# Kernel tuning notes

Hardware: AMD Instinct MI355X
Metric: run time of the kernel (lower is better)

The kernel has to match this reference:

```python
import math
import jax, jax.numpy as jnp
import numpy as np

EMB = 1024
HEADS = 16
HD = EMB // HEADS  # 64
MAXPOS = 1024
BATCH = 4
SEQ = 1024


def get_rope_cache(dim, max_pos, theta=10000.0):
    # NOTE: faithfully reproduces the (i - 1) quirk of the source (not the standard i)
    i = jnp.arange(dim // 2, dtype=jnp.float32)
    theta_i = theta ** (-2.0 * (i - 1.0) / dim)
    pos = jnp.arange(max_pos, dtype=jnp.float32)[:, None]
    th = pos * theta_i  # [max_pos, dim//2]
    return jnp.stack([jnp.cos(th), jnp.sin(th)], axis=-1)  # [max_pos, dim//2, 2]


def apply_rope(x, rope_cache):
    # x: [B, H, S, hd]. Source casts pairs to float16 before the complex multiply,
    # then the complex32*complex64 product promotes back to float32 -> emulate via
    # an fp16 round-trip on x, with the rotation itself done in fp32.
    B, H, S, hd = x.shape
    rc = rope_cache[:S]  # [S, hd//2, 2]
    xp = x.reshape(B, H, S, hd // 2, 2).astype(jnp.float16).astype(jnp.float32)
    a, b = xp[..., 0], xp[..., 1]
    cos, sin = rc[..., 0], rc[..., 1]
    rot = jnp.stack([a * cos - b * sin, a * sin + b * cos], axis=-1)
    return rot.reshape(B, H, S, hd)


def setup_inputs() -> dict:
    key = jax.random.key(0)
    ks = jax.random.split(key, 5)
    std = math.sqrt(2.0 / (EMB + EMB))
    x = jax.random.normal(ks[0], (BATCH, SEQ, EMB), dtype=jnp.float32)
    padding_mask = jnp.ones((BATCH, SEQ), dtype=jnp.float32)
    Wq = jax.random.normal(ks[1], (EMB, EMB), dtype=jnp.float32) * std
    Wk = jax.random.normal(ks[2], (EMB, EMB), dtype=jnp.float32) * std
    Wv = jax.random.normal(ks[3], (EMB, EMB), dtype=jnp.float32) * std
    Wo = jax.random.normal(ks[4], (EMB, EMB), dtype=jnp.float32) * std
    rope_cache = get_rope_cache(HD, MAXPOS)
    return {"x": x, "padding_mask": padding_mask, "Wq": Wq, "Wk": Wk,
            "Wv": Wv, "Wo": Wo, "rope_cache": rope_cache}


def reference(x, padding_mask, Wq, Wk, Wv, Wo, rope_cache):
    B, S, E = x.shape

    def heads(t):  # [B,S,E] -> [B,H,S,hd]
        return t.reshape(B, S, HEADS, HD).transpose(0, 2, 1, 3)

    q = heads(x @ Wq.T)
    k = heads(x @ Wk.T)
    v = heads(x @ Wv.T)
    q = apply_rope(q, rope_cache)
    k = apply_rope(k, rope_cache)

    scores = jnp.einsum('bhqd,bhkd->bhqk', q, k)  # [B,H,S,S]
    causal = jnp.tril(jnp.ones((S, S), jnp.float32))
    mask = (causal[None, :, :] * padding_mask[:, None, :])[:, None]  # [B,1,S,S]
    scores = jnp.where(mask == 0, jnp.float32(-1e9), scores) / math.sqrt(HD)
    weights = jax.nn.softmax(scores, axis=-1)

    out = jnp.einsum('bhqk,bhkd->bhqd', weights, v)  # [B,H,S,hd]
    # Faithful to source: transpose(-2,-1) then .view(B,S,-1) scrambles head_dim/seq
    out = out.transpose(0, 1, 3, 2).reshape(B, S, E)
    return out @ Wo.T
```

## Files before the change

### kernel.cpp

```cpp
#include <hip/hip_runtime.h>

#define SEQ   1024
#define HEADS 16
#define HD    64
#define BATCH 4
#define EMB   1024

typedef __attribute__((ext_vector_type(8))) short  short8;
typedef __attribute__((ext_vector_type(4))) float  floatx4;

__device__ __forceinline__ unsigned short f2bf(float f) {
    unsigned u = __builtin_bit_cast(unsigned, f);
    u += 0x7FFF + ((u >> 16) & 1);
    return (unsigned short)(u >> 16);
}

__device__ __forceinline__ void g2l16(const void* g, void* l) {
    __builtin_amdgcn_global_load_lds((const __attribute__((address_space(1))) unsigned int*)g,
                                     (__attribute__((address_space(3))) unsigned int*)l,
                                     16, 0, 0);
}

__device__ __forceinline__ short8 ldsfrag(const unsigned short* base, int row, int cq) {
    int ch = cq ^ (row & 7);
    return *(const short8*)(base + row * 64 + ch * 8);
}

__global__ __launch_bounds__(256) void cvt_kernel(
    const float* __restrict__ x,  const float* __restrict__ wq,
    const float* __restrict__ wk, const float* __restrict__ wv,
    const float* __restrict__ wo,
    unsigned short* __restrict__ xb,  unsigned short* __restrict__ wqb,
    unsigned short* __restrict__ wkb, unsigned short* __restrict__ wvb,
    unsigned short* __restrict__ wob) {
    int blk = blockIdx.x;
    const float* src; unsigned short* dst; int rel;
    if      (blk < 4096) { src = x;  dst = xb;  rel = blk; }
    else if (blk < 5120) { src = wq; dst = wqb; rel = blk - 4096; }
    else if (blk < 6144) { src = wk; dst = wkb; rel = blk - 5120; }
    else if (blk < 7168) { src = wv; dst = wvb; rel = blk - 6144; }
    else                 { src = wo; dst = wob; rel = blk - 7168; }
    size_t i = (size_t)rel * 1024 + threadIdx.x * 4;
    float4 v = *(const float4*)(src + i);
    ushort4 o;
    o.x = f2bf(v.x); o.y = f2bf(v.y); o.z = f2bf(v.z); o.w = f2bf(v.w);
    *(ushort4*)(dst + i) = o;
}

template<int MODE>
__global__ __launch_bounds__(256) void gemm_m97(
    const unsigned short* __restrict__ A, const unsigned short* __restrict__ W,
    void* __restrict__ out0, void* __restrict__ out1, void* __restrict__ out2,
    const float* __restrict__ rc, int M, int N, int K) {
    __shared__ unsigned short As[2][128 * 64];
    __shared__ unsigned short Bs[2][128 * 64];
    const int tid  = threadIdx.x;
    const int lane = tid & 63;
    const int wid  = tid >> 6;
    const int l15  = lane & 15, quad = lane >> 4;
    const int wm   = (wid & 1) * 64, wn = (wid >> 1) * 64;
    const int m0   = blockIdx.y * 128, n0 = blockIdx.x * 128;
    const int boff = tid * 16;

    floatx4 acc[4][4] = {};
    const char* Ab = (const char*)A;
    const char* Wb = (const char*)W;
    const size_t rstride = (size_t)K * 2;

    auto stageStep = [&](int bufi, int k0) {
#pragma unroll
        for (int c = 0; c < 4; c++) {
            int o = c * 4096 + boff;
            int row = o >> 7;
            int sw  = ((o >> 4) & 7) ^ (row & 7);
            g2l16(Ab + (size_t)(m0 + row) * rstride + (size_t)k0 * 2 + sw * 16,
                  (char*)As[bufi] + o);
            g2l16(Wb + (size_t)(n0 + row) * rstride + (size_t)k0 * 2 + sw * 16,
                  (char*)Bs[bufi] + o);
        }
    };

    stageStep(0, 0);
    __syncthreads();

    int cur = 0;
    for (int k0 = 0; k0 < K; k0 += 64) {
        if (k0 + 64 < K) stageStep(cur ^ 1, k0 + 64);

        const unsigned short* Ac = As[cur];
        const unsigned short* Bc = Bs[cur];
#pragma unroll
        for (int ks = 0; ks < 2; ks++) {
            short8 a[4], b[4];
#pragma unroll
            for (int i = 0; i < 4; i++) a[i] = ldsfrag(Ac, wm + i * 16 + l15, ks * 4 + quad);
#pragma unroll
            for (int j = 0; j < 4; j++) b[j] = ldsfrag(Bc, wn + j * 16 + l15, ks * 4 + quad);
#pragma unroll
            for (int i = 0; i < 4; i++)
#pragma unroll
                for (int j = 0; j < 4; j++)
                    acc[i][j] = __builtin_amdgcn_mfma_f32_16x16x32_bf16(a[i], b[j], acc[i][j], 0, 0, 0);
        }

        asm volatile("s_waitcnt vmcnt(0)" ::: "memory");
        __syncthreads();
        cur ^= 1;
    }

    const int which = n0 >> 10;
#pragma unroll
    for (int i = 0; i < 4; i++) {
#pragma unroll
        for (int r = 0; r < 4; r++) {
            int m = m0 + wm + i * 16 + quad * 4 + r;
            int bb = m >> 10, s = m & 1023;
#pragma unroll
            for (int j = 0; j < 4; j++) {
                int n = n0 + wn + j * 16 + l15;
                float v = acc[i][j][r];
                if (MODE == 0) {
                    ((float*)out0)[(size_t)m * N + n] = v;
                } else {
                    int nr = n & 1023, h = nr >> 6, d = nr & 63;
                    if (which < 2) {
                        float vp = __shfl_xor(v, 1);
                        float2 cs = *(const float2*)&rc[(size_t)s * 64 + (d & ~1)];
                        v = (l15 & 1) ? (vp * cs.y + v * cs.x) : (v * cs.x - vp * cs.y);
                        unsigned short* dst = (which == 0) ? (unsigned short*)out0
                                                           : (unsigned short*)out1;
                        dst[(((size_t)bb * HEADS + h) * SEQ + s) * HD + d] = f2bf(v);
                    } else {
                        ((unsigned short*)out2)[(((size_t)bb * HEADS + h) * HD + d) * SEQ + s] = f2bf(v);
                    }
                }
            }
        }
    }
}

__global__ __launch_bounds__(256) void gemm_proj64(
    const unsigned short* __restrict__ A, const unsigned short* __restrict__ W,
    float* __restrict__ out, int M, int N, int K) {
    __shared__ unsigned short As[2][64 * 64];
    __shared__ unsigned short Bs[2][128 * 64];
    const int tid  = threadIdx.x;
    const int lane = tid & 63;
    const int wid  = tid >> 6;
    const int l15  = lane & 15, quad = lane >> 4;
    const int wm   = (wid & 1) * 32, wn = (wid >> 1) * 64;
    const int m0   = blockIdx.y * 64, n0 = blockIdx.x * 128;
    const int boff = tid * 16;

    floatx4 acc[2][4] = {};
    const char* Ab = (const char*)A;
    const char* Wb = (const char*)W;
    const size_t rstride = (size_t)K * 2;

    auto stageStep = [&](int bufi, int k0) {
#pragma unroll
        for (int c = 0; c < 2; c++) {
            int o = c * 4096 + boff;
            int row = o >> 7;
            int sw  = ((o >> 4) & 7) ^ (row & 7);
            g2l16(Ab + (size_t)(m0 + row) * rstride + (size_t)k0 * 2 + sw * 16,
                  (char*)As[bufi] + o);
        }
#pragma unroll
        for (int c = 0; c < 4; c++) {
            int o = c * 4096 + boff;
            int row = o >> 7;
            int sw  = ((o >> 4) & 7) ^ (row & 7);
            g2l16(Wb + (size_t)(n0 + row) * rstride + (size_t)k0 * 2 + sw * 16,
                  (char*)Bs[bufi] + o);
        }
    };

    stageStep(0, 0);
    __syncthreads();

    int cur = 0;
    for (int k0 = 0; k0 < K; k0 += 64) {
        if (k0 + 64 < K) stageStep(cur ^ 1, k0 + 64);

        const unsigned short* Ac = As[cur];
        const unsigned short* Bc = Bs[cur];
#pragma unroll
        for (int ks = 0; ks < 2; ks++) {
            short8 a[2], b[4];
#pragma unroll
            for (int i = 0; i < 2; i++) a[i] = ldsfrag(Ac, wm + i * 16 + l15, ks * 4 + quad);
#pragma unroll
            for (int j = 0; j < 4; j++) b[j] = ldsfrag(Bc, wn + j * 16 + l15, ks * 4 + quad);
#pragma unroll
            for (int i = 0; i < 2; i++)
#pragma unroll
                for (int j = 0; j < 4; j++)
                    acc[i][j] = __builtin_amdgcn_mfma_f32_16x16x32_bf16(a[i], b[j], acc[i][j], 0, 0, 0);
        }

        asm volatile("s_waitcnt vmcnt(0)" ::: "memory");
        __syncthreads();
        cur ^= 1;
    }

#pragma unroll
    for (int i = 0; i < 2; i++) {
#pragma unroll
        for (int r = 0; r < 4; r++) {
            int m = m0 + wm + i * 16 + quad * 4 + r;
#pragma unroll
            for (int j = 0; j < 4; j++) {
                int n = n0 + wn + j * 16 + l15;
                out[(size_t)m * N + n] = acc[i][j][r];
            }
        }
    }
}

__global__ __launch_bounds__(256) void attn_kernel(
    const unsigned short* __restrict__ Qb, const unsigned short* __restrict__ Kb,
    const unsigned short* __restrict__ VTb, const float* __restrict__ pm,
    unsigned short* __restrict__ Tb) {
    __shared__ unsigned short Ks[2][64 * 64];
    __shared__ unsigned short Vs[2][64 * 64];
    const int tid  = threadIdx.x;
    const int lane = tid & 63, wid = tid >> 6;
    const int l15  = lane & 15, quad = lane >> 4;
    const int bh   = blockIdx.x, b = bh >> 4;
    const int q0   = (15 - blockIdx.y) * 64;
    const int qw   = q0 + wid * 16;
    const int q    = qw + l15;
    const unsigned short* Qh  = Qb  + (size_t)bh * SEQ * HD;
    const unsigned short* Kh  = Kb  + (size_t)bh * SEQ * HD;
    const unsigned short* VTh = VTb + (size_t)bh * HD * SEQ;
    unsigned short*       Th  = Tb  + (size_t)bh * HD * SEQ;
    const float* pmb = pm + b * SEQ;
    const float SCL2 = 0.125f * 1.44269504088896340736f;

    short8 qf0 = *(const short8*)&Qh[(size_t)q * HD + quad * 8];
    short8 qf1 = *(const short8*)&Qh[(size_t)q * HD + 32 + quad * 8];

    floatx4 ot[4] = {};
    float l_lane = 0.f;
    const int boff = tid * 16;
    const int srcA = l15 + ((quad & 1) << 5);
    const int srcB = srcA + 16;
    const bool hi  = (quad >> 1) & 1;

    auto stageKV = [&](int bufi, int kvc) {
        const char* kg = (const char*)(Kh + (size_t)kvc * HD);
        const char* vg = (const char*)(VTh + kvc);
#pragma unroll
        for (int c = 0; c < 2; c++) {
            int o = c * 4096 + boff;
            int row = o >> 7;
            int sw  = ((o >> 4) & 7) ^ (row & 7);
            g2l16(kg + (size_t)row * 128 + sw * 16, (char*)Ks[bufi] + o);
            g2l16(vg + (size_t)row * (SEQ * 2) + sw * 16, (char*)Vs[bufi] + o);
        }
    };

    stageKV(0, 0);
    __syncthreads();

    int cur = 0;
    for (int kvc = 0; kvc <= q0; kvc += 64) {
        if (kvc + 64 <= q0) stageKV(cur ^ 1, kvc + 64);

        const unsigned short* Kc = Ks[cur];
        const unsigned short* Vc = Vs[cur];
        const bool diag = (kvc + 63 > qw);
        floatx4 sc[4];
#pragma unroll
        for (int st = 0; st < 4; st++) {
            short8 ka0 = ldsfrag(Kc, st * 16 + l15, quad);
            short8 ka1 = ldsfrag(Kc, st * 16 + l15, 4 + quad);
            floatx4 z = {0.f, 0.f, 0.f, 0.f};
            z = __builtin_amdgcn_mfma_f32_16x16x32_bf16(ka0, qf0, z, 0, 0, 0);
            z = __builtin_amdgcn_mfma_f32_16x16x32_bf16(ka1, qf1, z, 0, 0, 0);
            sc[st] = z;
        }
        unsigned w0[4], w1[4];
#pragma unroll
        for (int st = 0; st < 4; st++) {
            int kvbase = kvc + st * 16 + quad * 4;
            float4 pmv = *(const float4*)&pmb[kvbase];
            float p[4];
#pragma unroll
            for (int r = 0; r < 4; r++) {
                float e = exp2f(sc[st][r] * SCL2) * (((&pmv.x)[r] != 0.f) ? 1.f : 0.f);
                if (diag && (kvbase + r > q)) e = 0.f;
                l_lane += e;
                p[r] = e;
            }
            w0[st] = (unsigned)f2bf(p[0]) | ((unsigned)f2bf(p[1]) << 16);
            w1[st] = (unsigned)f2bf(p[2]) | ((unsigned)f2bf(p[3]) << 16);
        }
        unsigned a0 = __shfl(w0[0], srcA), a1 = __shfl(w0[1], srcA);
        unsigned b0 = __shfl(w1[0], srcA), b1 = __shfl(w1[1], srcA);
        unsigned c0 = __shfl(w0[0], srcB), c1 = __shfl(w0[1], srcB);
        unsigned d0 = __shfl(w1[0], srcB), d1 = __shfl(w1[1], srcB);
        uint4 f0 = { hi ? a1 : a0, hi ? b1 : b0, hi ? c1 : c0, hi ? d1 : d0 };
        short8 pf0 = __builtin_bit_cast(short8, f0);
        a0 = __shfl(w0[2], srcA); a1 = __shfl(w0[3], srcA);
        b0 = __shfl(w1[2], srcA); b1 = __shfl(w1[3], srcA);
        c0 = __shfl(w0[2], srcB); c1 = __shfl(w0[3], srcB);
        d0 = __shfl(w1[2], srcB); d1 = __shfl(w1[3], srcB);
        uint4 f1 = { hi ? a1 : a0, hi ? b1 : b0, hi ? c1 : c0, hi ? d1 : d0 };
        short8 pf1 = __builtin_bit_cast(short8, f1);

#pragma unroll
        for (int jt = 0; jt < 4; jt++) {
            short8 v0 = ldsfrag(Vc, jt * 16 + l15, quad);
            short8 v1 = ldsfrag(Vc, jt * 16 + l15, 4 + quad);
            ot[jt] = __builtin_amdgcn_mfma_f32_16x16x32_bf16(v0, pf0, ot[jt], 0, 0, 0);
            ot[jt] = __builtin_amdgcn_mfma_f32_16x16x32_bf16(v1, pf1, ot[jt], 0, 0, 0);
        }

        asm volatile("s_waitcnt vmcnt(0)" ::: "memory");
        __syncthreads();
        cur ^= 1;
    }

    float l = l_lane;
    l += __shfl_xor(l, 16);
    l += __shfl_xor(l, 32);
    float inv = 1.0f / l;
#pragma unroll
    for (int jt = 0; jt < 4; jt++)
#pragma unroll
        for (int r = 0; r < 4; r++)
            Th[(size_t)(jt * 16 + quad * 4 + r) * SEQ + q] = f2bf(ot[jt][r] * inv);
}

extern "C" void kernel_launch(void* const* d_in, const int* in_sizes, int n_in,
                              void* d_out, int out_size, void* d_ws, size_t ws_size,
                              hipStream_t stream) {
    const float* x  = (const float*)d_in[0];
    const float* pm = (const float*)d_in[1];
    const float* Wq = (const float*)d_in[2];
    const float* Wk = (const float*)d_in[3];
    const float* Wv = (const float*)d_in[4];
    const float* Wo = (const float*)d_in[5];
    const float* rc = (const float*)d_in[6];

    char* base = (char*)d_ws;
    unsigned short* xb   = (unsigned short*)(base);
    unsigned short* wqkv = (unsigned short*)(base + (8u  << 20));
    unsigned short* wob  = (unsigned short*)(base + (14u << 20));
    unsigned short* Qb   = (unsigned short*)(base + (16u << 20));
    unsigned short* Kb   = (unsigned short*)(base + (24u << 20));
    unsigned short* VTb  = (unsigned short*)(base + (32u << 20));
    unsigned short* Tb   = (unsigned short*)(base + (40u << 20));

    cvt_kernel<<<8192, 256, 0, stream>>>(x, Wq, Wk, Wv, Wo,
                                         xb, wqkv, wqkv + (1u << 20), wqkv + (2u << 20), wob);
    gemm_m97<1><<<dim3(24, 32), 256, 0, stream>>>(xb, wqkv, (void*)Qb, (void*)Kb, (void*)VTb,
                                                  rc, 4096, 3072, 1024);
    attn_kernel<<<dim3(64, 16), 256, 0, stream>>>(Qb, Kb, VTb, pm, Tb);
    gemm_proj64<<<dim3(8, 64), 256, 0, stream>>>(Tb, wob, (float*)d_out, 4096, 1024, 1024);
}
```

Before: 199.0 us.

## Pre-pack weights into MFMA fragment order and load B directly to registers

The conversion kernel now writes Wq/Wk/Wv/Wo in bf16, packed per 128x64 tile in the exact per-lane MFMA B-fragment order. Both GEMMs then load B fragments straight from global memory into registers, dropping the B shared-memory buffers and their LDS reads. The QKV GEMM also remaps block IDs across 8 groups, likely to spread work over XCDs for better L2 locality. The trade-off is that B global loads now sit on the critical path each k-step with no software double buffering. Less LDS use may allow higher occupancy.

```diff
diff --git a/kernel.cpp b/kernel.cpp
--- a/kernel.cpp
+++ b/kernel.cpp
@@ -30,44 +30,74 @@
     const float* __restrict__ x,  const float* __restrict__ wq,
     const float* __restrict__ wk, const float* __restrict__ wv,
     const float* __restrict__ wo,
-    unsigned short* __restrict__ xb,  unsigned short* __restrict__ wqb,
-    unsigned short* __restrict__ wkb, unsigned short* __restrict__ wvb,
-    unsigned short* __restrict__ wob) {
+    unsigned short* __restrict__ xb, unsigned short* __restrict__ wqkvP,
+    unsigned short* __restrict__ woP) {
     int blk = blockIdx.x;
-    const float* src; unsigned short* dst; int rel;
-    if      (blk < 4096) { src = x;  dst = xb;  rel = blk; }
-    else if (blk < 5120) { src = wq; dst = wqb; rel = blk - 4096; }
-    else if (blk < 6144) { src = wk; dst = wkb; rel = blk - 5120; }
-    else if (blk < 7168) { src = wv; dst = wvb; rel = blk - 6144; }
-    else                 { src = wo; dst = wob; rel = blk - 7168; }
-    size_t i = (size_t)rel * 1024 + threadIdx.x * 4;
-    float4 v = *(const float4*)(src + i);
-    ushort4 o;
-    o.x = f2bf(v.x); o.y = f2bf(v.y); o.z = f2bf(v.z); o.w = f2bf(v.w);
-    *(ushort4*)(dst + i) = o;
-}
-
-template<int MODE>
-__global__ __launch_bounds__(256) void gemm_m97(
-    const unsigned short* __restrict__ A, const unsigned short* __restrict__ W,
-    void* __restrict__ out0, void* __restrict__ out1, void* __restrict__ out2,
-    const float* __restrict__ rc, int M, int N, int K) {
+    int tid = threadIdx.x;
+    if (blk < 4096) {
+        size_t i = (size_t)blk * 1024 + tid * 4;
+        float4 v = *(const float4*)(x + i);
+        ushort4 o;
+        o.x = f2bf(v.x); o.y = f2bf(v.y); o.z = f2bf(v.z); o.w = f2bf(v.w);
+        *(ushort4*)(xb + i) = o;
+        return;
+    }
+    int pblk = blk - 4096;
+    const float* src; unsigned short* dst; int n0t, kt;
+    if (pblk < 384) {
+        n0t = pblk >> 4; kt = pblk & 15;
+        int which = n0t >> 3;
+        src = (which == 0) ? wq : (which == 1) ? wk : wv;
+        src += (size_t)(n0t & 7) * 128 * 1024;
+        dst = wqkvP + (size_t)pblk * 8192;
+    } else {
+        int p2 = pblk - 384;
+        n0t = p2 >> 4; kt = p2 & 15;
+        src = wo + (size_t)n0t * 128 * 1024;
+        dst = woP + (size_t)p2 * 8192;
+    }
+#pragma unroll
+    for (int s = 0; s < 4; s++) {
+        int w    = tid * 4 + s;
+        int ks   = w >> 9, jj = (w >> 6) & 7, lane = w & 63;
+        int row  = jj * 16 + (lane & 15);
+        int col  = kt * 64 + ks * 32 + (lane >> 4) * 8;
+        const float* sp = src + (size_t)row * 1024 + col;
+        float4 v0 = *(const float4*)sp;
+        float4 v1 = *(const float4*)(sp + 4);
+        ushort4 o0, o1;
+        o0.x = f2bf(v0.x); o0.y = f2bf(v0.y); o0.z = f2bf(v0.z); o0.w = f2bf(v0.w);
+        o1.x = f2bf(v1.x); o1.y = f2bf(v1.y); o1.z = f2bf(v1.z); o1.w = f2bf(v1.w);
+        *(ushort4*)(dst + (size_t)w * 8)     = o0;
+        *(ushort4*)(dst + (size_t)w * 8 + 4) = o1;
+    }
+}
+
+__global__ __launch_bounds__(256) void gemm_qkv(
+    const unsigned short* __restrict__ A, const unsigned short* __restrict__ Wp,
+    unsigned short* __restrict__ outQ, unsigned short* __restrict__ outK,
+    unsigned short* __restrict__ outV, const float* __restrict__ rc,
+    int M, int N, int K) {
     __shared__ unsigned short As[2][128 * 64];
-    __shared__ unsigned short Bs[2][128 * 64];
     const int tid  = threadIdx.x;
     const int lane = tid & 63;
     const int wid  = tid >> 6;
     const int l15  = lane & 15, quad = lane >> 4;
     const int wm   = (wid & 1) * 64, wn = (wid >> 1) * 64;
-    const int m0   = blockIdx.y * 128, n0 = blockIdx.x * 128;
+    const int nbx  = gridDim.x;
+    const int cpx  = (nbx * gridDim.y) >> 3;
+    const int bid  = blockIdx.y * nbx + blockIdx.x;
+    const int virt = (bid & 7) * cpx + (bid >> 3);
+    const int n0t  = virt % nbx;
+    const int m0   = (virt / nbx) * 128, n0 = n0t * 128;
     const int boff = tid * 16;
 
     floatx4 acc[4][4] = {};
     const char* Ab = (const char*)A;
-    const char* Wb = (const char*)W;
     const size_t rstride = (size_t)K * 2;
-
-    auto stageStep = [&](int bufi, int k0) {
+    const unsigned short* wpb = Wp + ((size_t)(wn >> 4) * 64 + lane) * 8;
+
+    auto stageA = [&](int bufi, int k0) {
 #pragma unroll
         for (int c = 0; c < 4; c++) {
             int o = c * 4096 + boff;
@@ -75,34 +105,37 @@
             int sw  = ((o >> 4) & 7) ^ (row & 7);
             g2l16(Ab + (size_t)(m0 + row) * rstride + (size_t)k0 * 2 + sw * 16,
                   (char*)As[bufi] + o);
-            g2l16(Wb + (size_t)(n0 + row) * rstride + (size_t)k0 * 2 + sw * 16,
-                  (char*)Bs[bufi] + o);
         }
     };
 
-    stageStep(0, 0);
+    stageA(0, 0);
     __syncthreads();
 
     int cur = 0;
     for (int k0 = 0; k0 < K; k0 += 64) {
-        if (k0 + 64 < K) stageStep(cur ^ 1, k0 + 64);
+        const int kt = k0 >> 6;
+        const unsigned short* wp = wpb + (size_t)(n0t * 16 + kt) * 8192;
+        short8 b8[2][4];
+#pragma unroll
+        for (int ks = 0; ks < 2; ks++)
+#pragma unroll
+            for (int j = 0; j < 4; j++)
+                b8[ks][j] = *(const short8*)(wp + (ks * 512 + j * 64) * 8);
+        __builtin_amdgcn_sched_barrier(0);
+        if (k0 + 64 < K) stageA(cur ^ 1, k0 + 64);
 
         const unsigned short* Ac = As[cur];
-        const unsigned short* Bc = Bs[cur];
 #pragma unroll
         for (int ks = 0; ks < 2; ks++) {
-            short8 a[4], b[4];
+            short8 a[4];
 #pragma unroll
             for (int i = 0; i < 4; i++) a[i] = ldsfrag(Ac, wm + i * 16 + l15, ks * 4 + quad);
 #pragma unroll
-            for (int j = 0; j < 4; j++) b[j] = ldsfrag(Bc, wn + j * 16 + l15, ks * 4 + quad);
-#pragma unroll
             for (int i = 0; i < 4; i++)
 #pragma unroll
                 for (int j = 0; j < 4; j++)
-                    acc[i][j] = __builtin_amdgcn_mfma_f32_16x16x32_bf16(a[i], b[j], acc[i][j], 0, 0, 0);
-        }
-
+                    acc[i][j] = __builtin_amdgcn_mfma_f32_16x16x32_bf16(a[i], b8[ks][j], acc[i][j], 0, 0, 0);
+        }
         asm volatile("s_waitcnt vmcnt(0)" ::: "memory");
         __syncthreads();
         cur ^= 1;
@@ -119,20 +152,15 @@
             for (int j = 0; j < 4; j++) {
                 int n = n0 + wn + j * 16 + l15;
                 float v = acc[i][j][r];
-                if (MODE == 0) {
-                    ((float*)out0)[(size_t)m * N + n] = v;
+                int nr = n & 1023, h = nr >> 6, d = nr & 63;
+                if (which < 2) {
+                    float vp = __shfl_xor(v, 1);
+                    float2 cs = *(const float2*)&rc[(size_t)s * 64 + (d & ~1)];
+                    v = (l15 & 1) ? (vp * cs.y + v * cs.x) : (v * cs.x - vp * cs.y);
+                    unsigned short* dst = (which == 0) ? outQ : outK;
+                    dst[(((size_t)bb * HEADS + h) * SEQ + s) * HD + d] = f2bf(v);
                 } else {
-                    int nr = n & 1023, h = nr >> 6, d = nr & 63;
-                    if (which < 2) {
-                        float vp = __shfl_xor(v, 1);
-                        float2 cs = *(const float2*)&rc[(size_t)s * 64 + (d & ~1)];
-                        v = (l15 & 1) ? (vp * cs.y + v * cs.x) : (v * cs.x - vp * cs.y);
-                        unsigned short* dst = (which == 0) ? (unsigned short*)out0
-                                                           : (unsigned short*)out1;
-                        dst[(((size_t)bb * HEADS + h) * SEQ + s) * HD + d] = f2bf(v);
-                    } else {
-                        ((unsigned short*)out2)[(((size_t)bb * HEADS + h) * HD + d) * SEQ + s] = f2bf(v);
-                    }
+                    outV[(((size_t)bb * HEADS + h) * HD + d) * SEQ + s] = f2bf(v);
                 }
             }
         }
@@ -140,24 +168,24 @@
 }
 
 __global__ __launch_bounds__(256) void gemm_proj64(
-    const unsigned short* __restrict__ A, const unsigned short* __restrict__ W,
+    const unsigned short* __restrict__ A, const unsigned short* __restrict__ Wp,
     float* __restrict__ out, int M, int N, int K) {
     __shared__ unsigned short As[2][64 * 64];
-    __shared__ unsigned short Bs[2][128 * 64];
     const int tid  = threadIdx.x;
     const int lane = tid & 63;
     const int wid  = tid >> 6;
     const int l15  = lane & 15, quad = lane >> 4;
     const int wm   = (wid & 1) * 32, wn = (wid >> 1) * 64;
-    const int m0   = blockIdx.y * 64, n0 = blockIdx.x * 128;
+    const int n0t  = blockIdx.x;
+    const int m0   = blockIdx.y * 64, n0 = n0t * 128;
     const int boff = tid * 16;
 
     floatx4 acc[2][4] = {};
     const char* Ab = (const char*)A;
-    const char* Wb = (const char*)W;
     const size_t rstride = (size_t)K * 2;
-
-    auto stageStep = [&](int bufi, int k0) {
+    const unsigned short* wpb = Wp + ((size_t)(wn >> 4) * 64 + lane) * 8;
+
+    auto stageA = [&](int bufi, int k0) {
 #pragma unroll
         for (int c = 0; c < 2; c++) {
             int o = c * 4096 + boff;
@@ -166,39 +194,36 @@
             g2l16(Ab + (size_t)(m0 + row) * rstride + (size_t)k0 * 2 + sw * 16,
                   (char*)As[bufi] + o);
         }
-#pragma unroll
-        for (int c = 0; c < 4; c++) {
-            int o = c * 4096 + boff;
-            int row = o >> 7;
-            int sw  = ((o >> 4) & 7) ^ (row & 7);
-            g2l16(Wb + (size_t)(n0 + row) * rstride + (size_t)k0 * 2 + sw * 16,
-                  (char*)Bs[bufi] + o);
-        }
     };
 
-    stageStep(0, 0);
+    stageA(0, 0);
     __syncthreads();
 
     int cur = 0;
     for (int k0 = 0; k0 < K; k0 += 64) {
-        if (k0 + 64 < K) stageStep(cur ^ 1, k0 + 64);
+        const int kt = k0 >> 6;
+        const unsigned short* wp = wpb + (size_t)(n0t * 16 + kt) * 8192;
+        short8 b8[2][4];
+#pragma unroll
+        for (int ks = 0; ks < 2; ks++)
+#pragma unroll
+            for (int j = 0; j < 4; j++)
+                b8[ks][j] = *(const short8*)(wp + (ks * 512 + j * 64) * 8);
+        __builtin_amdgcn_sched_barrier(0);
+        if (k0 + 64 < K) stageA(cur ^ 1, k0 + 64);
 
         const unsigned short* Ac = As[cur];
-        const unsigned short* Bc = Bs[cur];
 #pragma unroll
         for (int ks = 0; ks < 2; ks++) {
-            short8 a[2], b[4];
+            short8 a[2];
 #pragma unroll
             for (int i = 0; i < 2; i++) a[i] = ldsfrag(Ac, wm + i * 16 + l15, ks * 4 + quad);
 #pragma unroll
-            for (int j = 0; j < 4; j++) b[j] = ldsfrag(Bc, wn + j * 16 + l15, ks * 4 + quad);
-#pragma unroll
             for (int i = 0; i < 2; i++)
 #pragma unroll
                 for (int j = 0; j < 4; j++)
-                    acc[i][j] = __builtin_amdgcn_mfma_f32_16x16x32_bf16(a[i], b[j], acc[i][j], 0, 0, 0);
-        }
-
+                    acc[i][j] = __builtin_amdgcn_mfma_f32_16x16x32_bf16(a[i], b8[ks][j], acc[i][j], 0, 0, 0);
+        }
         asm volatile("s_waitcnt vmcnt(0)" ::: "memory");
         __syncthreads();
         cur ^= 1;
@@ -346,18 +371,17 @@
     const float* rc = (const float*)d_in[6];
 
     char* base = (char*)d_ws;
-    unsigned short* xb   = (unsigned short*)(base);
-    unsigned short* wqkv = (unsigned short*)(base + (8u  << 20));
-    unsigned short* wob  = (unsigned short*)(base + (14u << 20));
-    unsigned short* Qb   = (unsigned short*)(base + (16u << 20));
-    unsigned short* Kb   = (unsigned short*)(base + (24u << 20));
-    unsigned short* VTb  = (unsigned short*)(base + (32u << 20));
-    unsigned short* Tb   = (unsigned short*)(base + (40u << 20));
-
-    cvt_kernel<<<8192, 256, 0, stream>>>(x, Wq, Wk, Wv, Wo,
-                                         xb, wqkv, wqkv + (1u << 20), wqkv + (2u << 20), wob);
-    gemm_m97<1><<<dim3(24, 32), 256, 0, stream>>>(xb, wqkv, (void*)Qb, (void*)Kb, (void*)VTb,
-                                                  rc, 4096, 3072, 1024);
+    unsigned short* xb    = (unsigned short*)(base);
+    unsigned short* wqkvP = (unsigned short*)(base + (8u  << 20));
+    unsigned short* woP   = (unsigned short*)(base + (14u << 20));
+    unsigned short* Qb    = (unsigned short*)(base + (16u << 20));
+    unsigned short* Kb    = (unsigned short*)(base + (24u << 20));
+    unsigned short* VTb   = (unsigned short*)(base + (32u << 20));
+    unsigned short* Tb    = (unsigned short*)(base + (40u << 20));
+
+    cvt_kernel<<<4608, 256, 0, stream>>>(x, Wq, Wk, Wv, Wo, xb, wqkvP, woP);
+    gemm_qkv<<<dim3(24, 32), 256, 0, stream>>>(xb, wqkvP, Qb, Kb, VTb,
+                                               rc, 4096, 3072, 1024);
     attn_kernel<<<dim3(64, 16), 256, 0, stream>>>(Qb, Kb, VTb, pm, Tb);
-    gemm_proj64<<<dim3(8, 64), 256, 0, stream>>>(Tb, wob, (float*)d_out, 4096, 1024, 1024);
-}
+    gemm_proj64<<<dim3(8, 64), 256, 0, stream>>>(Tb, woP, (float*)d_out, 4096, 1024, 1024);
+}
```

Measured after the change: 194.1 us. 1.03x faster.
